# Kernel tuning notes

Hardware: AMD Instinct MI355X
Metric: run time of the kernel (lower is better)

Reference implementation:

```python
import jax, jax.numpy as jnp
import numpy as np
from jax import lax

B, D, N = 1024, 1024, 65536
M, Ks, DS = 8, 256, 128      # key PQ: subvectors, codewords, subvec dim (D/M)
MV, DV = 8, 256              # value PQ: subvectors, subvec dim (OUT/MV)
OUT = MV * DV
K_TOP = 64


def setup_inputs() -> dict:
    key = jax.random.key(0)
    ks = jax.random.split(key, 7)
    x = jax.random.normal(ks[0], (B, D), dtype=jnp.float32)
    # whitening matrix starts as identity in the module; perturb slightly for a non-trivial test
    whitening_matrix = jnp.eye(D, dtype=jnp.float32) + 0.01 * jax.random.normal(ks[1], (D, D), dtype=jnp.float32)
    key_codebooks = jax.random.normal(ks[2], (M, Ks, DS), dtype=jnp.float32)
    value_codebooks = jax.random.normal(ks[3], (MV, Ks, DV), dtype=jnp.float32)
    bias = jnp.zeros((OUT,), dtype=jnp.float32)
    key_codes = jax.random.randint(ks[4], (N, M), 0, Ks, dtype=jnp.int32)
    value_codes = jax.random.randint(ks[5], (N, MV), 0, Ks, dtype=jnp.int32)
    return {
        "x": x,
        "whitening_matrix": whitening_matrix,
        "key_codebooks": key_codebooks,
        "value_codebooks": value_codebooks,
        "bias": bias,
        "key_codes": key_codes,
        "value_codes": value_codes,
        "k": K_TOP,
    }


def reference(x, whitening_matrix, key_codebooks, value_codebooks, bias, key_codes, value_codes, k):
    # 1) whiten the query (module buffer 'whitening_matrix')
    q = x @ whitening_matrix                      # [B, D]
    qs = q.reshape(B, M, DS)                      # [B, M, DS] query subvectors

    # 2) ADC distance tables: squared L2 between each query subvector and each codeword
    #    dt[b, m, c] = ||qs[b,m] - cb[m,c]||^2
    q_sq = jnp.sum(qs * qs, axis=-1)              # [B, M]
    c_sq = jnp.sum(key_codebooks * key_codebooks, axis=-1)  # [M, Ks]
    cross = jnp.einsum("bmd,mcd->bmc", qs, key_codebooks)   # [B, M, Ks]
    dt = q_sq[:, :, None] + c_sq[None, :, :] - 2.0 * cross  # [B, M, Ks]

    # 3) asymmetric distance to all N stored keys via code gather (irregular access)
    lut = dt.transpose(1, 0, 2)                   # [M, B, Ks]
    # per-subvector gather then sum: d[b, n] = sum_m lut[m, b, key_codes[n, m]]
    dists = jax.vmap(lambda l, c: l[:, c])(lut, key_codes.T).sum(axis=0)  # [B, N]

    # 4) top-k nearest neighbors
    neg_top, top_idx = lax.top_k(-dists, k)       # [B, k]

    # 5) reconstruct values of retrieved neighbors from value PQ codebooks
    vc = value_codes[top_idx]                     # [B, k, MV] int codes
    vals = value_codebooks[jnp.arange(MV)[None, None, :], vc]  # [B, k, MV, DV]
    vals = vals.reshape(vals.shape[0], vals.shape[1], OUT)      # [B, k, OUT]

    # 6) distance-weighted aggregation (softmax over negative distances) + bias
    w = jax.nn.softmax(neg_top, axis=-1)          # [B, k]
    y = jnp.einsum("bk,bko->bo", w, vals) + bias  # [B, OUT]
    return y
```

## Files before the change

### kernel.cpp

```cpp
#include <hip/hip_runtime.h>

#define N_ITEMS 65536

__launch_bounds__(256)
__global__ void gemm_q_kernel(const float* __restrict__ A,
                              const float* __restrict__ W,
                              float* __restrict__ qpart) {
  __shared__ float As[16][132];
  __shared__ float Bs[16][132];
  const int tid = threadIdx.x;
  const int tx = tid & 15, ty = tid >> 4;
  const int rb = blockIdx.y * 128, cb = blockIdx.x * 128;
  const int kz = blockIdx.z * 128;
  const int ar = tid >> 2, ac = (tid & 3) << 2;
  const int bk = tid >> 5, bc = (tid & 31) << 2;

  float4 va0 = *(const float4*)&A[(rb + ar) * 1024 + kz + ac];
  float4 va1 = *(const float4*)&A[(rb + ar + 64) * 1024 + kz + ac];
  float4 vb0 = *(const float4*)&W[(kz + bk) * 1024 + cb + bc];
  float4 vb1 = *(const float4*)&W[(kz + bk + 8) * 1024 + cb + bc];

  float acc[8][8] = {};
  for (int k0 = 0; k0 < 128; k0 += 16) {
    As[ac + 0][ar] = va0.x; As[ac + 1][ar] = va0.y;
    As[ac + 2][ar] = va0.z; As[ac + 3][ar] = va0.w;
    As[ac + 0][ar + 64] = va1.x; As[ac + 1][ar + 64] = va1.y;
    As[ac + 2][ar + 64] = va1.z; As[ac + 3][ar + 64] = va1.w;
    *(float4*)&Bs[bk][bc] = vb0;
    *(float4*)&Bs[bk + 8][bc] = vb1;
    __syncthreads();
    if (k0 + 16 < 128) {
      va0 = *(const float4*)&A[(rb + ar) * 1024 + kz + k0 + 16 + ac];
      va1 = *(const float4*)&A[(rb + ar + 64) * 1024 + kz + k0 + 16 + ac];
      vb0 = *(const float4*)&W[(kz + k0 + 16 + bk) * 1024 + cb + bc];
      vb1 = *(const float4*)&W[(kz + k0 + 16 + bk + 8) * 1024 + cb + bc];
    }
#pragma unroll
    for (int kk = 0; kk < 16; kk++) {
      const float4 a0 = *(const float4*)&As[kk][ty << 2];
      const float4 a1 = *(const float4*)&As[kk][64 + (ty << 2)];
      const float4 b0 = *(const float4*)&Bs[kk][tx << 2];
      const float4 b1 = *(const float4*)&Bs[kk][64 + (tx << 2)];
      const float ar8[8] = {a0.x, a0.y, a0.z, a0.w, a1.x, a1.y, a1.z, a1.w};
      const float br8[8] = {b0.x, b0.y, b0.z, b0.w, b1.x, b1.y, b1.z, b1.w};
#pragma unroll
      for (int r = 0; r < 8; r++)
#pragma unroll
        for (int c = 0; c < 8; c++)
          acc[r][c] = fmaf(ar8[r], br8[c], acc[r][c]);
    }
    __syncthreads();
  }
  float* outp = qpart + blockIdx.z * 1048576;
#pragma unroll
  for (int rh = 0; rh < 2; rh++)
#pragma unroll
    for (int r = 0; r < 4; r++) {
      const int row = rb + rh * 64 + (ty << 2) + r;
      const int ri = rh * 4 + r;
      *(float4*)&outp[row * 1024 + cb + (tx << 2)] =
          make_float4(acc[ri][0], acc[ri][1], acc[ri][2], acc[ri][3]);
      *(float4*)&outp[row * 1024 + cb + 64 + (tx << 2)] =
          make_float4(acc[ri][4], acc[ri][5], acc[ri][6], acc[ri][7]);
    }
}

__launch_bounds__(256)
__global__ void qsum_kernel(const float4* __restrict__ qp,
                            float4* __restrict__ q) {
  const int i = blockIdx.x * 256 + threadIdx.x;
  float4 s0 = qp[i];
  float4 s1 = qp[i + 131072];
#pragma unroll
  for (int z = 1; z < 8; z++) {
    const float4 a = qp[z * 262144 + i];
    const float4 b = qp[z * 262144 + i + 131072];
    s0.x += a.x; s0.y += a.y; s0.z += a.z; s0.w += a.w;
    s1.x += b.x; s1.y += b.y; s1.z += b.z; s1.w += b.w;
  }
  q[i] = s0;
  q[i + 131072] = s1;
}

__launch_bounds__(256)
__global__ void lut_kernel(const float* __restrict__ q,
                           const float* __restrict__ kcb,
                           const int* __restrict__ key_codes,
                           float* __restrict__ lut,
                           unsigned long long* __restrict__ pcodes,
                           uint4* __restrict__ poffs) {
  if (blockIdx.z == 8) {
    const int g0 = (((int)blockIdx.y * 4 + (int)blockIdx.x) * 256 + (int)threadIdx.x) * 4;
#pragma unroll
    for (int t = 0; t < 4; t++) {
      const int gid = g0 + t;
      unsigned long long p = 0ull;
      unsigned h[8];
#pragma unroll
      for (int j = 0; j < 8; j++) {
        const unsigned c = (unsigned)key_codes[gid * 8 + j] & 255u;
        p |= (unsigned long long)c << (8 * j);
        h[j] = c << 6;
      }
      pcodes[gid] = p;
      poffs[gid] = make_uint4(h[0] | (h[1] << 16), h[2] | (h[3] << 16),
                              h[4] | (h[5] << 16), h[6] | (h[7] << 16));
    }
    return;
  }

  __shared__ float As[32][68];
  __shared__ float Bs[32][68];
  const int tid = threadIdx.x;
  const int tx = tid & 15, ty = tid >> 4;
  const int m = blockIdx.z;
  const int rb = blockIdx.y * 64;
  const int cb0 = blockIdx.x * 64;
  float acc[4][4] = {};
  float qa[4] = {}, cs[4] = {};
  for (int k0 = 0; k0 < 128; k0 += 32) {
#pragma unroll
    for (int l = 0; l < 2; l++) {
      const int e = tid + l * 256;
      const int row = e >> 3, c4 = (e & 7) << 2;
      const float4 va = *(const float4*)&q[(rb + row) * 1024 + m * 128 + k0 + c4];
      As[c4 + 0][row] = va.x; As[c4 + 1][row] = va.y;
      As[c4 + 2][row] = va.z; As[c4 + 3][row] = va.w;
      const float4 vb = *(const float4*)&kcb[(m * 256 + cb0 + row) * 128 + k0 + c4];
      Bs[c4 + 0][row] = vb.x; Bs[c4 + 1][row] = vb.y;
      Bs[c4 + 2][row] = vb.z; Bs[c4 + 3][row] = vb.w;
    }
    __syncthreads();
#pragma unroll
    for (int kk = 0; kk < 32; kk++) {
      const float4 a = *(const float4*)&As[kk][ty << 2];
      const float4 b = *(const float4*)&Bs[kk][tx << 2];
      const float ar[4] = {a.x, a.y, a.z, a.w};
      const float br[4] = {b.x, b.y, b.z, b.w};
#pragma unroll
      for (int r = 0; r < 4; r++)
#pragma unroll
        for (int c = 0; c < 4; c++)
          acc[r][c] = fmaf(ar[r], br[c], acc[r][c]);
#pragma unroll
      for (int r = 0; r < 4; r++) qa[r] = fmaf(ar[r], ar[r], qa[r]);
#pragma unroll
      for (int c = 0; c < 4; c++) cs[c] = fmaf(br[c], br[c], cs[c]);
    }
    __syncthreads();
  }
#pragma unroll
  for (int r = 0; r < 4; r++) {
    const int row = rb + (ty << 2) + r;
    const int col = cb0 + (tx << 2);
    float4 v;
    v.x = qa[r] + cs[0] - 2.0f * acc[r][0];
    v.y = qa[r] + cs[1] - 2.0f * acc[r][1];
    v.z = qa[r] + cs[2] - 2.0f * acc[r][2];
    v.w = qa[r] + cs[3] - 2.0f * acc[r][3];
    *(float4*)&lut[row * 2048 + m * 256 + col] = v;
  }
}

extern __shared__ char dyn_lds[];

__launch_bounds__(1024)
__global__ void scansel_kernel(const float* __restrict__ lutf,
                               const uint4* __restrict__ poffs,
                               const unsigned long long* __restrict__ pcodes,
                               const int* __restrict__ value_codes,
                               const float* __restrict__ vcb,
                               const float* __restrict__ bias,
                               float* __restrict__ out) {
  char* repb = dyn_lds;
  unsigned char* temps = (unsigned char*)(dyn_lds + 131072);
  unsigned* tempw = (unsigned*)(dyn_lds + 131072);
  const int tid = threadIdx.x;
  const int g = blockIdx.x;

  {
    const int w = tid >> 6, lane = tid & 63;
#pragma unroll
    for (int t0 = 0; t0 < 2; t0++) {
      const int t = w + t0 * 16;
      const int rr = t & 3, seg = t >> 2;
      const int row = (g << 2) + rr;
      const int e0 = seg * 256 + lane * 4;
      const float4 v4 = *(const float4*)&lutf[row * 2048 + e0];
      float s4 = v4.x + v4.y + v4.z + v4.w;
#pragma unroll
      for (int off = 32; off > 0; off >>= 1) s4 += __shfl_xor(s4, off);
      const float mean = s4 * (1.0f / 256.0f);
      const float vals[4] = {v4.x, v4.y, v4.z, v4.w};
#pragma unroll
      for (int k = 0; k < 4; k++) {
        int iv = (int)rintf(vals[k] - mean);
        iv = max(-127, min(127, iv));
        temps[(e0 + k) * 4 + rr] = (unsigned char)(iv + 128);
      }
    }
  }
  __syncthreads();

  {
    const int lane = tid & 63;
    const unsigned v0 = tempw[tid * 2];
    const unsigned v1 = tempw[tid * 2 + 1];
    const uint4 q0 = make_uint4(v0, v0, v0, v0);
    const uint4 q1 = make_uint4(v1, v1, v1, v1);
    uint4* repv = (uint4*)dyn_lds;
#pragma unroll
    for (int k = 0; k < 4; k++) {
      const int kk = (k + lane) & 3;
      repv[tid * 8 + kk] = q0;
      repv[tid * 8 + 4 + kk] = q1;
    }
  }
  __syncthreads();

  const int r = tid & 15;
  const char* base0 = repb + (r << 2);
  const char* base1 = repb + 65536 + (r << 2);
  unsigned k0[4], k1[4];
#pragma unroll
  for (int j = 0; j < 4; j++) { k0[j] = 0xFFFFFFFFu; k1[j] = 0xFFFFFFFFu; }

  unsigned A[8], B[8];

  auto issue = [&](unsigned (&BUF)[8], const uint4 cw) {
    BUF[0] = *(const unsigned*)(base0 + (cw.x & 0xFFFFu));
    BUF[1] = *(const unsigned*)(base0 + (cw.x >> 16) + 16384);
    BUF[2] = *(const unsigned*)(base0 + (cw.y & 0xFFFFu) + 32768);
    BUF[3] = *(const unsigned*)(base0 + (cw.y >> 16) + 49152);
    BUF[4] = *(const unsigned*)(base1 + (cw.z & 0xFFFFu));
    BUF[5] = *(const unsigned*)(base1 + (cw.z >> 16) + 16384);
    BUF[6] = *(const unsigned*)(base1 + (cw.w & 0xFFFFu) + 32768);
    BUF[7] = *(const unsigned*)(base1 + (cw.w >> 16) + 49152);
  };

  auto consume = [&](const unsigned (&BUF)[8], const int it) {
    const unsigned M = 0x00FF00FFu;
    unsigned accA = BUF[0] & M;
    unsigned accB = (BUF[0] >> 8) & M;
#pragma unroll
    for (int j = 1; j < 8; j++) {
      accA += BUF[j] & M;
      accB += (BUF[j] >> 8) & M;
    }
    const int ss[4] = {(int)(accA & 0xFFFFu), (int)(accB & 0xFFFFu),
                       (int)(accA >> 16), (int)(accB >> 16)};
#pragma unroll
    for (int j = 0; j < 4; j++) {
      const unsigned key = ((unsigned)ss[j] << 6) | (unsigned)it;
      const unsigned mx = (k0[j] > key) ? k0[j] : key;
      k0[j] = (k0[j] < key) ? k0[j] : key;
      k1[j] = (k1[j] < mx) ? k1[j] : mx;
    }
  };

  {
    const uint4 cA = poffs[tid];
    issue(A, cA);
  }
  uint4 cNxt = poffs[tid + 1024];

  for (int it = 0; it < 64; it += 2) {
    const uint4 c2 = poffs[tid + (((it + 2) & 63) << 10)];
    const uint4 c3 = poffs[tid + (((it + 3) & 63) << 10)];
    issue(B, cNxt);
    consume(A, it);
    issue(A, c2);
    consume(B, it + 1);
    cNxt = c3;
  }

  __syncthreads();

  unsigned* cl  = (unsigned*)dyn_lds;
  float* wts    = (float*)(dyn_lds + 4096);
  unsigned long long* sv8 = (unsigned long long*)(dyn_lds + 8192);
  float* gred   = (float*)(dyn_lds + 16384);
  unsigned* rmin = (unsigned*)(dyn_lds + 16448);
  int* rcnt     = (int*)(dyn_lds + 16464);
  float* rws    = (float*)(dyn_lds + 16480);

  if (tid < 4) { rmin[tid] = 0xFFFFFFFFu; rcnt[tid] = 0; }
  __syncthreads();

#pragma unroll
  for (int j = 0; j < 4; j++) {
    unsigned d = k0[j] >> 6;
#pragma unroll
    for (int off = 32; off > 0; off >>= 1) {
      const unsigned o = __shfl_xor(d, off);
      d = (o < d) ? o : d;
    }
    if ((tid & 63) == 0) atomicMin(&rmin[j], d);
  }
  __syncthreads();

  {
    const int lane = tid & 63;
    const unsigned long long lm = (1ull << lane) - 1ull;
#pragma unroll
    for (int j = 0; j < 4; j++) {
      const unsigned lim = rmin[j] + 20u;
#pragma unroll
      for (int c = 0; c < 2; c++) {
        const unsigned key = c ? k1[j] : k0[j];
        const unsigned d = key >> 6;
        const bool pred = d <= lim;
        const unsigned long long m = __ballot(pred);
        int base = 0;
        if (lane == 0 && m) base = atomicAdd(&rcnt[j], __popcll(m));
        base = __shfl(base, 0);
        if (pred) {
          const int pos = base + __popcll(m & lm);
          if (pos < 256)
            cl[j * 256 + pos] = (d << 16) | ((key & 63u) << 10) | (unsigned)tid;
        }
      }
    }
  }
  __syncthreads();

  const int gj = tid >> 8, gt = tid & 255;
  const int cnt_g = min(rcnt[gj], 256);
  float dex = 1e30f;
  if (gt < cnt_g) {
    const unsigned pc = cl[gj * 256 + gt];
    const int n = (int)(pc & 0xFFFFu);
    const unsigned long long c8 = pcodes[n];
    const uint4 vc0 = *(const uint4*)&value_codes[n * 8];
    const uint4 vc1 = *(const uint4*)&value_codes[n * 8 + 4];
    sv8[gj * 256 + gt] =
        (unsigned long long)(vc0.x & 255u)        | ((unsigned long long)(vc0.y & 255u) << 8)  |
        ((unsigned long long)(vc0.z & 255u) << 16) | ((unsigned long long)(vc0.w & 255u) << 24) |
        ((unsigned long long)(vc1.x & 255u) << 32) | ((unsigned long long)(vc1.y & 255u) << 40) |
        ((unsigned long long)(vc1.z & 255u) << 48) | ((unsigned long long)(vc1.w & 255u) << 56);
    const float* lrow = lutf + ((g << 2) + gj) * 2048;
    const unsigned lo = (unsigned)c8, hi = (unsigned)(c8 >> 32);
    dex  = lrow[        (lo       & 255u)];
    dex += lrow[ 256 + ((lo >>  8) & 255u)];
    dex += lrow[ 512 + ((lo >> 16) & 255u)];
    dex += lrow[ 768 + ((lo >> 24)       )];
    dex += lrow[1024 + ( hi        & 255u)];
    dex += lrow[1280 + ((hi >>  8) & 255u)];
    dex += lrow[1536 + ((hi >> 16) & 255u)];
    dex += lrow[1792 + ((hi >> 24)       )];
  }
  float mnf = dex;
#pragma unroll
  for (int off = 32; off > 0; off >>= 1) mnf = fminf(mnf, __shfl_xor(mnf, off));
  if ((tid & 63) == 0) gred[gj * 4 + ((tid >> 6) & 3)] = mnf;
  __syncthreads();
  const float dminx = fminf(fminf(gred[gj * 4], gred[gj * 4 + 1]),
                            fminf(gred[gj * 4 + 2], gred[gj * 4 + 3]));
  const float w = (gt < cnt_g) ? __expf(dminx - dex) : 0.f;
  wts[gj * 256 + gt] = w;
  float sw_ = w;
#pragma unroll
  for (int off = 32; off > 0; off >>= 1) sw_ += __shfl_xor(sw_, off);
  __syncthreads();
  if ((tid & 63) == 0) gred[gj * 4 + ((tid >> 6) & 3)] = sw_;
  __syncthreads();
  if (gt == 0)
    rws[gj] = 1.0f / (gred[gj * 4] + gred[gj * 4 + 1] + gred[gj * 4 + 2] + gred[gj * 4 + 3]);
  __syncthreads();

  const int h = tid >> 9, u = tid & 511;
  const int col = u << 2;
  const int mv = col >> 8;
  const int co = col & 255;
  const float* vb2 = vcb + mv * 65536 + co;
  const float4 bb = *(const float4*)&bias[col];
#pragma unroll
  for (int jr = 0; jr < 2; jr++) {
    const int j = (jr << 1) | h;
    const int row = (g << 2) + j;
    const int cj = min(rcnt[j], 256);
    float4 acc = make_float4(0.f, 0.f, 0.f, 0.f);
    int k = 0;
    for (; k + 1 < cj; k += 2) {
      const float w0 = wts[j * 256 + k];
      const float w1 = wts[j * 256 + k + 1];
      const unsigned c0 = (unsigned)((sv8[j * 256 + k] >> (mv * 8)) & 255ull);
      const unsigned c1 = (unsigned)((sv8[j * 256 + k + 1] >> (mv * 8)) & 255ull);
      const float4 v0 = *(const float4*)(vb2 + c0 * 256);
      const float4 v1 = *(const float4*)(vb2 + c1 * 256);
      acc.x = fmaf(w0, v0.x, acc.x); acc.y = fmaf(w0, v0.y, acc.y);
      acc.z = fmaf(w0, v0.z, acc.z); acc.w = fmaf(w0, v0.w, acc.w);
      acc.x = fmaf(w1, v1.x, acc.x); acc.y = fmaf(w1, v1.y, acc.y);
      acc.z = fmaf(w1, v1.z, acc.z); acc.w = fmaf(w1, v1.w, acc.w);
    }
    if (k < cj) {
      const float w0 = wts[j * 256 + k];
      const unsigned c0 = (unsigned)((sv8[j * 256 + k] >> (mv * 8)) & 255ull);
      const float4 v0 = *(const float4*)(vb2 + c0 * 256);
      acc.x = fmaf(w0, v0.x, acc.x); acc.y = fmaf(w0, v0.y, acc.y);
      acc.z = fmaf(w0, v0.z, acc.z); acc.w = fmaf(w0, v0.w, acc.w);
    }
    const float iv = rws[j];
    *(float4*)&out[row * 2048 + col] =
        make_float4(fmaf(acc.x, iv, bb.x), fmaf(acc.y, iv, bb.y),
                    fmaf(acc.z, iv, bb.z), fmaf(acc.w, iv, bb.w));
  }
}

__launch_bounds__(512)
__global__ void scan16_kernel(const float* __restrict__ lut,
                              const unsigned long long* __restrict__ pcodes,
                              unsigned* __restrict__ cand_d,
                              unsigned short* __restrict__ cand_n) {
  __shared__ short sRep[32768];
  const int tid = threadIdx.x;
  const int b = blockIdx.x;

  const float4 v4 = *(const float4*)&lut[b * 2048 + tid * 4];
  float s4 = v4.x + v4.y + v4.z + v4.w;
#pragma unroll
  for (int off = 32; off > 0; off >>= 1) s4 += __shfl_xor(s4, off);
  const float mean = s4 * (1.0f / 256.0f);

  const float vals[4] = {v4.x, v4.y, v4.z, v4.w};
#pragma unroll
  for (int k2 = 0; k2 < 4; k2++) {
    float f = (vals[k2] - mean) * 64.0f;
    f = fmaxf(fminf(f, 32000.0f), -32000.0f);
    const int iv = (int)rintf(f);
    const unsigned hw = (unsigned)(unsigned short)iv;
    const unsigned wrd = hw | (hw << 16);
    const uint4 wv = make_uint4(wrd, wrd, wrd, wrd);
    const int e = tid * 4 + k2;
    *(uint4*)&((unsigned*)sRep)[e * 8] = wv;
    *(uint4*)&((unsigned*)sRep)[e * 8 + 4] = wv;
  }
  __syncthreads();

  const int r = tid & 15;
  int d0 = 0x7FFFFFFF, d1 = 0x7FFFFFFF, d2 = 0x7FFFFFFF, d3 = 0x7FFFFFFF;
  int i0 = 0, i1 = 0, i2 = 0, i3 = 0;

  unsigned long long c8 = pcodes[tid];
  for (int it = 0; it < 128; it++) {
    const int n = tid + (it << 9);
    unsigned long long nxt = 0ull;
    if (it < 127) nxt = pcodes[n + 512];
    const unsigned lo = (unsigned)c8;
    const unsigned hi = (unsigned)(c8 >> 32);
    int s;
    s  = sRep[(((lo      ) & 255u) << 4) + r        ];
    s += sRep[(((lo >>  8) & 255u) << 4) + r +  4096];
    s += sRep[(((lo >> 16) & 255u) << 4) + r +  8192];
    s += sRep[(((lo >> 24)       ) << 4) + r + 12288];
    s += sRep[(((hi      ) & 255u) << 4) + r + 16384];
    s += sRep[(((hi >>  8) & 255u) << 4) + r + 20480];
    s += sRep[(((hi >> 16) & 255u) << 4) + r + 24576];
    s += sRep[(((hi >> 24)       ) << 4) + r + 28672];
    if (s < d3) {
      if (s < d1) {
        if (s < d0) { d3 = d2; i3 = i2; d2 = d1; i2 = i1; d1 = d0; i1 = i0; d0 = s; i0 = n; }
        else        { d3 = d2; i3 = i2; d2 = d1; i2 = i1; d1 = s; i1 = n; }
      } else {
        if (s < d2) { d3 = d2; i3 = i2; d2 = s; i2 = n; }
        else        { d3 = s; i3 = n; }
      }
    }
    c8 = nxt;
  }

  const int base = b * 2048 + tid * 4;
  const uint4 dv = make_uint4((unsigned)(d0 + 0x40000000), (unsigned)(d1 + 0x40000000),
                              (unsigned)(d2 + 0x40000000), (unsigned)(d3 + 0x40000000));
  *(uint4*)&cand_d[base] = dv;
  const unsigned ni01 = (unsigned)i0 | ((unsigned)i1 << 16);
  const unsigned ni23 = (unsigned)i2 | ((unsigned)i3 << 16);
  *(uint2*)&cand_n[base] = make_uint2(ni01, ni23);
}

__launch_bounds__(256)
__global__ void select_kernel(const unsigned* __restrict__ cand_d,
                              const unsigned short* __restrict__ cand_n,
                              const int* __restrict__ value_codes,
                              const float* __restrict__ vcb,
                              const float* __restrict__ bias,
                              const unsigned long long* __restrict__ pcodes,
                              const float* __restrict__ lutf,
                              const unsigned lim_add,
                              float* __restrict__ out) {
  __shared__ unsigned sredw[4];
  __shared__ float sredf[4];
  __shared__ unsigned long long clist[256];
  __shared__ float sw[256];
  __shared__ int svc[2048];
  __shared__ int scnt;
  __shared__ float sWsum;

  const int tid = threadIdx.x;
  const int b = blockIdx.x;

  const uint4 a0 = *(const uint4*)&cand_d[b * 2048 + tid * 8];
  const uint4 a1 = *(const uint4*)&cand_d[b * 2048 + tid * 8 + 4];
  const uint4 nn = *(const uint4*)&cand_n[b * 2048 + tid * 8];
  unsigned dk[8] = {a0.x, a0.y, a0.z, a0.w, a1.x, a1.y, a1.z, a1.w};
  unsigned ni[8] = {nn.x & 0xFFFFu, nn.x >> 16, nn.y & 0xFFFFu, nn.y >> 16,
                    nn.z & 0xFFFFu, nn.z >> 16, nn.w & 0xFFFFu, nn.w >> 16};

  if (tid == 0) scnt = 0;
  unsigned mn = dk[0];
#pragma unroll
  for (int j = 1; j < 8; j++) mn = (dk[j] < mn) ? dk[j] : mn;
#pragma unroll
  for (int off = 32; off > 0; off >>= 1) {
    const unsigned o = __shfl_xor(mn, off);
    mn = (o < mn) ? o : mn;
  }
  if ((tid & 63) == 0) sredw[tid >> 6] = mn;
  __syncthreads();
  unsigned sMin = sredw[0];
  sMin = (sredw[1] < sMin) ? sredw[1] : sMin;
  sMin = (sredw[2] < sMin) ? sredw[2] : sMin;
  sMin = (sredw[3] < sMin) ? sredw[3] : sMin;
  const unsigned lim = sMin + lim_add;

  const int lane = tid & 63;
  const unsigned long long lm = (1ull << lane) - 1ull;
#pragma unroll
  for (int j = 0; j < 8; j++) {
    const bool pred = dk[j] <= lim;
    const unsigned long long mask = __ballot(pred);
    int base = 0;
    if (lane == 0 && mask) base = atomicAdd(&scnt, __popcll(mask));
    base = __shfl(base, 0);
    if (pred) {
      const int pos = base + __popcll(mask & lm);
      if (pos < 256) clist[pos] = ((unsigned long long)dk[j] << 32) | ni[j];
    }
  }
  __syncthreads();
  const int cnt = min(scnt, 256);

  float dex = 1e30f;
  if (tid < cnt) {
    const int n = (int)(clist[tid] & 0xFFFFFFFFu);
    const unsigned long long c8 = pcodes[n];
    const float* lrow = lutf + b * 2048;
    const unsigned lo = (unsigned)c8, hi = (unsigned)(c8 >> 32);
    dex  = lrow[        (lo       & 255u)];
    dex += lrow[ 256 + ((lo >>  8) & 255u)];
    dex += lrow[ 512 + ((lo >> 16) & 255u)];
    dex += lrow[ 768 + ((lo >> 24)       )];
    dex += lrow[1024 + ( hi        & 255u)];
    dex += lrow[1280 + ((hi >>  8) & 255u)];
    dex += lrow[1536 + ((hi >> 16) & 255u)];
    dex += lrow[1792 + ((hi >> 24)       )];
  }
  for (int i = tid; i < (cnt << 3); i += 256)
    svc[i] = value_codes[((int)(clist[i >> 3] & 0xFFFFFFFFu)) * 8 + (i & 7)];
  float mnf = dex;
#pragma unroll
  for (int off = 32; off > 0; off >>= 1) mnf = fminf(mnf, __shfl_xor(mnf, off));
  if ((tid & 63) == 0) sredf[tid >> 6] = mnf;
  __syncthreads();
  const float dminx = fminf(fminf(sredf[0], sredf[1]), fminf(sredf[2], sredf[3]));
  if (tid < cnt) sw[tid] = __expf(dminx - dex);
  __syncthreads();

  if (tid < 64) {
    float s = 0.f;
    for (int j = tid; j < cnt; j += 64) s += sw[j];
#pragma unroll
    for (int off = 32; off > 0; off >>= 1) s += __shfl_xor(s, off);
    if (tid == 0) sWsum = s;
  }
  __syncthreads();
  const float inv = 1.0f / sWsum;

  const int c0 = tid << 3;
  const int mv = c0 >> 8;
  const int off = c0 & 255;
  float4 acc0 = make_float4(0.f, 0.f, 0.f, 0.f);
  float4 acc1 = make_float4(0.f, 0.f, 0.f, 0.f);
  const float* vbase = vcb + mv * 65536 + off;
  for (int k = 0; k < cnt; k++) {
    const float w = sw[k];
    const float* vp = vbase + svc[(k << 3) + mv] * 256;
    const float4 v0 = *(const float4*)vp;
    const float4 v1 = *(const float4*)(vp + 4);
    acc0.x = fmaf(w, v0.x, acc0.x); acc0.y = fmaf(w, v0.y, acc0.y);
    acc0.z = fmaf(w, v0.z, acc0.z); acc0.w = fmaf(w, v0.w, acc0.w);
    acc1.x = fmaf(w, v1.x, acc1.x); acc1.y = fmaf(w, v1.y, acc1.y);
    acc1.z = fmaf(w, v1.z, acc1.z); acc1.w = fmaf(w, v1.w, acc1.w);
  }
  const float4 b0 = *(const float4*)&bias[c0];
  const float4 b1 = *(const float4*)&bias[c0 + 4];
  *(float4*)&out[b * 2048 + c0] =
      make_float4(fmaf(acc0.x, inv, b0.x), fmaf(acc0.y, inv, b0.y),
                  fmaf(acc0.z, inv, b0.z), fmaf(acc0.w, inv, b0.w));
  *(float4*)&out[b * 2048 + c0 + 4] =
      make_float4(fmaf(acc1.x, inv, b1.x), fmaf(acc1.y, inv, b1.y),
                  fmaf(acc1.z, inv, b1.z), fmaf(acc1.w, inv, b1.w));
}

extern "C" void kernel_launch(void* const* d_in, const int* in_sizes, int n_in,
                              void* d_out, int out_size, void* d_ws, size_t ws_size,
                              hipStream_t stream) {
  const float* x    = (const float*)d_in[0];
  const float* W    = (const float*)d_in[1];
  const float* kcb  = (const float*)d_in[2];
  const float* vcb  = (const float*)d_in[3];
  const float* bias = (const float*)d_in[4];
  const int* key_codes   = (const int*)d_in[5];
  const int* value_codes = (const int*)d_in[6];
  float* out = (float*)d_out;

  float* qpart = (float*)d_ws;
  float* q     = qpart + 8388608;
  float* lut   = q + 1048576;
  uint4* poffs = (uint4*)(lut + 2097152);
  unsigned long long* pcodes = (unsigned long long*)(poffs + 65536);
  unsigned* cand_d = (unsigned*)d_ws;
  unsigned short* cand_n = (unsigned short*)(cand_d + 2097152);

  hipLaunchKernelGGL(gemm_q_kernel, dim3(8, 8, 8), dim3(256), 0, stream,
                     x, W, qpart);
  hipLaunchKernelGGL(qsum_kernel, dim3(512), dim3(256), 0, stream,
                     (const float4*)qpart, (float4*)q);
  hipLaunchKernelGGL(lut_kernel, dim3(4, 16, 9), dim3(256), 0, stream,
                     q, kcb, key_codes, lut, pcodes, poffs);

  const hipError_t attr_rc = hipFuncSetAttribute(
      (const void*)scansel_kernel, hipFuncAttributeMaxDynamicSharedMemorySize, 139264);
  if (attr_rc == hipSuccess) {
    hipLaunchKernelGGL(scansel_kernel, dim3(256), dim3(1024), 139264, stream,
                       lut, poffs, pcodes, value_codes, vcb, bias, out);
  } else {
    hipLaunchKernelGGL(scan16_kernel, dim3(1024), dim3(512), 0, stream,
                       lut, pcodes, cand_d, cand_n);
    hipLaunchKernelGGL(select_kernel, dim3(1024), dim3(256), 0, stream,
                       cand_d, cand_n, value_codes, vcb, bias, pcodes, lut,
                       1024u, out);
  }
}
```

Baseline: 165.9 us.

## Split scan over two halves of keys per block and merge with softmax combine

```diff
diff --git a/kernel.cpp b/kernel.cpp
--- a/kernel.cpp
+++ b/kernel.cpp
@@ -100,7 +100,7 @@
       for (int j = 0; j < 8; j++) {
         const unsigned c = (unsigned)key_codes[gid * 8 + j] & 255u;
         p |= (unsigned long long)c << (8 * j);
-        h[j] = c << 6;
+        h[j] = c * 36u;
       }
       pcodes[gid] = p;
       poffs[gid] = make_uint4(h[0] | (h[1] << 16), h[2] | (h[3] << 16),
@@ -170,13 +170,14 @@
                                const unsigned long long* __restrict__ pcodes,
                                const int* __restrict__ value_codes,
                                const float* __restrict__ vcb,
-                               const float* __restrict__ bias,
-                               float* __restrict__ out) {
+                               float* __restrict__ partials,
+                               float2* __restrict__ mW) {
   char* repb = dyn_lds;
-  unsigned char* temps = (unsigned char*)(dyn_lds + 131072);
-  unsigned* tempw = (unsigned*)(dyn_lds + 131072);
+  unsigned char* temps = (unsigned char*)(dyn_lds + 73728);
+  unsigned* tempw = (unsigned*)(dyn_lds + 73728);
   const int tid = threadIdx.x;
-  const int g = blockIdx.x;
+  const int g = blockIdx.x >> 1;
+  const int hf = blockIdx.x & 1;
 
   {
     const int w = tid >> 6, lane = tid & 63;
@@ -203,24 +204,21 @@
   __syncthreads();
 
   {
-    const int lane = tid & 63;
     const unsigned v0 = tempw[tid * 2];
     const unsigned v1 = tempw[tid * 2 + 1];
-    const uint4 q0 = make_uint4(v0, v0, v0, v0);
-    const uint4 q1 = make_uint4(v1, v1, v1, v1);
-    uint4* repv = (uint4*)dyn_lds;
-#pragma unroll
-    for (int k = 0; k < 4; k++) {
-      const int kk = (k + lane) & 3;
-      repv[tid * 8 + kk] = q0;
-      repv[tid * 8 + 4 + kk] = q1;
-    }
-  }
-  __syncthreads();
-
-  const int r = tid & 15;
+    unsigned* repw = (unsigned*)dyn_lds;
+    const int d0 = tid * 18;
+#pragma unroll
+    for (int r2 = 0; r2 < 8; r2++) {
+      repw[d0 + r2] = v0;
+      repw[d0 + 9 + r2] = v1;
+    }
+  }
+  __syncthreads();
+
+  const int r = tid & 7;
   const char* base0 = repb + (r << 2);
-  const char* base1 = repb + 65536 + (r << 2);
+  const char* base1 = repb + 36864 + (r << 2);
   unsigned k0[4], k1[4];
 #pragma unroll
   for (int j = 0; j < 4; j++) { k0[j] = 0xFFFFFFFFu; k1[j] = 0xFFFFFFFFu; }
@@ -229,13 +227,13 @@
 
   auto issue = [&](unsigned (&BUF)[8], const uint4 cw) {
     BUF[0] = *(const unsigned*)(base0 + (cw.x & 0xFFFFu));
-    BUF[1] = *(const unsigned*)(base0 + (cw.x >> 16) + 16384);
-    BUF[2] = *(const unsigned*)(base0 + (cw.y & 0xFFFFu) + 32768);
-    BUF[3] = *(const unsigned*)(base0 + (cw.y >> 16) + 49152);
+    BUF[1] = *(const unsigned*)(base0 + (cw.x >> 16) + 9216);
+    BUF[2] = *(const unsigned*)(base0 + (cw.y & 0xFFFFu) + 18432);
+    BUF[3] = *(const unsigned*)(base0 + (cw.y >> 16) + 27648);
     BUF[4] = *(const unsigned*)(base1 + (cw.z & 0xFFFFu));
-    BUF[5] = *(const unsigned*)(base1 + (cw.z >> 16) + 16384);
-    BUF[6] = *(const unsigned*)(base1 + (cw.w & 0xFFFFu) + 32768);
-    BUF[7] = *(const unsigned*)(base1 + (cw.w >> 16) + 49152);
+    BUF[5] = *(const unsigned*)(base1 + (cw.z >> 16) + 9216);
+    BUF[6] = *(const unsigned*)(base1 + (cw.w & 0xFFFFu) + 18432);
+    BUF[7] = *(const unsigned*)(base1 + (cw.w >> 16) + 27648);
   };
 
   auto consume = [&](const unsigned (&BUF)[8], const int it) {
@@ -258,15 +256,16 @@
     }
   };
 
+  const int nb = (hf << 15) + tid;
   {
-    const uint4 cA = poffs[tid];
+    const uint4 cA = poffs[nb];
     issue(A, cA);
   }
-  uint4 cNxt = poffs[tid + 1024];
-
-  for (int it = 0; it < 64; it += 2) {
-    const uint4 c2 = poffs[tid + (((it + 2) & 63) << 10)];
-    const uint4 c3 = poffs[tid + (((it + 3) & 63) << 10)];
+  uint4 cNxt = poffs[nb + 1024];
+
+  for (int it = 0; it < 32; it += 2) {
+    const uint4 c2 = poffs[nb + (((it + 2) & 31) << 10)];
+    const uint4 c3 = poffs[nb + (((it + 3) & 31) << 10)];
     issue(B, cNxt);
     consume(A, it);
     issue(A, c2);
@@ -282,7 +281,8 @@
   float* gred   = (float*)(dyn_lds + 16384);
   unsigned* rmin = (unsigned*)(dyn_lds + 16448);
   int* rcnt     = (int*)(dyn_lds + 16464);
-  float* rws    = (float*)(dyn_lds + 16480);
+  float* dmin4  = (float*)(dyn_lds + 16480);
+  float* wsum4  = (float*)(dyn_lds + 16496);
 
   if (tid < 4) { rmin[tid] = 0xFFFFFFFFu; rcnt[tid] = 0; }
   __syncthreads();
@@ -329,7 +329,7 @@
   float dex = 1e30f;
   if (gt < cnt_g) {
     const unsigned pc = cl[gj * 256 + gt];
-    const int n = (int)(pc & 0xFFFFu);
+    const int n = (hf << 15) + (int)(pc & 0xFFFFu);
     const unsigned long long c8 = pcodes[n];
     const uint4 vc0 = *(const uint4*)&value_codes[n * 8];
     const uint4 vc1 = *(const uint4*)&value_codes[n * 8 + 4];
@@ -364,19 +364,23 @@
   __syncthreads();
   if ((tid & 63) == 0) gred[gj * 4 + ((tid >> 6) & 3)] = sw_;
   __syncthreads();
-  if (gt == 0)
-    rws[gj] = 1.0f / (gred[gj * 4] + gred[gj * 4 + 1] + gred[gj * 4 + 2] + gred[gj * 4 + 3]);
-  __syncthreads();
-
-  const int h = tid >> 9, u = tid & 511;
+  if (gt == 0) {
+    dmin4[gj] = dminx;
+    wsum4[gj] = gred[gj * 4] + gred[gj * 4 + 1] + gred[gj * 4 + 2] + gred[gj * 4 + 3];
+  }
+  __syncthreads();
+
+  if (tid < 4)
+    mW[((g << 2) + tid) * 2 + hf] = make_float2(dmin4[tid], wsum4[tid]);
+
+  const int hp = tid >> 9, u = tid & 511;
   const int col = u << 2;
   const int mv = col >> 8;
   const int co = col & 255;
   const float* vb2 = vcb + mv * 65536 + co;
-  const float4 bb = *(const float4*)&bias[col];
 #pragma unroll
   for (int jr = 0; jr < 2; jr++) {
-    const int j = (jr << 1) | h;
+    const int j = (jr << 1) | hp;
     const int row = (g << 2) + j;
     const int cj = min(rcnt[j], 256);
     float4 acc = make_float4(0.f, 0.f, 0.f, 0.f);
@@ -400,10 +404,37 @@
       acc.x = fmaf(w0, v0.x, acc.x); acc.y = fmaf(w0, v0.y, acc.y);
       acc.z = fmaf(w0, v0.z, acc.z); acc.w = fmaf(w0, v0.w, acc.w);
     }
-    const float iv = rws[j];
-    *(float4*)&out[row * 2048 + col] =
-        make_float4(fmaf(acc.x, iv, bb.x), fmaf(acc.y, iv, bb.y),
-                    fmaf(acc.z, iv, bb.z), fmaf(acc.w, iv, bb.w));
+    *(float4*)&partials[((row << 1) + hf) * 2048 + col] = acc;
+  }
+}
+
+__launch_bounds__(256)
+__global__ void combine_kernel(const float* __restrict__ partials,
+                               const float2* __restrict__ mW,
+                               const float* __restrict__ bias,
+                               float* __restrict__ out) {
+  const int row = blockIdx.x;
+  const int t = threadIdx.x;
+  const float2 mw0 = mW[row * 2];
+  const float2 mw1 = mW[row * 2 + 1];
+  const float m = fminf(mw0.x, mw1.x);
+  const float a0 = __expf(m - mw0.x);
+  const float a1 = __expf(m - mw1.x);
+  const float inv = 1.0f / fmaf(a0, mw0.y, a1 * mw1.y);
+  const int c = t * 8;
+  const float* p0 = partials + (row * 2) * 2048 + c;
+  const float* p1 = partials + (row * 2 + 1) * 2048 + c;
+#pragma unroll
+  for (int v = 0; v < 2; v++) {
+    const float4 x0 = *(const float4*)(p0 + v * 4);
+    const float4 x1 = *(const float4*)(p1 + v * 4);
+    const float4 bb = *(const float4*)&bias[c + v * 4];
+    float4 o;
+    o.x = fmaf(fmaf(a0, x0.x, a1 * x1.x), inv, bb.x);
+    o.y = fmaf(fmaf(a0, x0.y, a1 * x1.y), inv, bb.y);
+    o.z = fmaf(fmaf(a0, x0.z, a1 * x1.z), inv, bb.z);
+    o.w = fmaf(fmaf(a0, x0.w, a1 * x1.w), inv, bb.w);
+    *(float4*)&out[row * 2048 + c + v * 4] = o;
   }
 }
 
@@ -619,6 +650,8 @@
   float* lut   = q + 1048576;
   uint4* poffs = (uint4*)(lut + 2097152);
   unsigned long long* pcodes = (unsigned long long*)(poffs + 65536);
+  float* partials = (float*)(pcodes + 65536);
+  float2* mW = (float2*)(partials + 4194304);
   unsigned* cand_d = (unsigned*)d_ws;
   unsigned short* cand_n = (unsigned short*)(cand_d + 2097152);
 
@@ -630,10 +663,12 @@
                      q, kcb, key_codes, lut, pcodes, poffs);
 
   const hipError_t attr_rc = hipFuncSetAttribute(
-      (const void*)scansel_kernel, hipFuncAttributeMaxDynamicSharedMemorySize, 139264);
+      (const void*)scansel_kernel, hipFuncAttributeMaxDynamicSharedMemorySize, 81920);
   if (attr_rc == hipSuccess) {
-    hipLaunchKernelGGL(scansel_kernel, dim3(256), dim3(1024), 139264, stream,
-                       lut, poffs, pcodes, value_codes, vcb, bias, out);
+    hipLaunchKernelGGL(scansel_kernel, dim3(512), dim3(1024), 81920, stream,
+                       lut, poffs, pcodes, value_codes, vcb, partials, mW);
+    hipLaunchKernelGGL(combine_kernel, dim3(1024), dim3(256), 0, stream,
+                       partials, mW, bias, out);
   } else {
     hipLaunchKernelGGL(scan16_kernel, dim3(1024), dim3(512), 0, stream,
                        lut, pcodes, cand_d, cand_n);
```

Result: slower. 172.0 us (+3.6%).
